# Optimization experiments

Hardware: AMD Instinct MI355X
Metric: run time of the kernel (lower is better)

The kernel has to match this reference:

```python
import jax, jax.numpy as jnp
import numpy as np

C = 128; D_INNER = 256; D_STATE = 16; D_CONV = 4; DT_RANK = 8; SCALE_MLP = 2


def layernorm(x, g, b, eps=1e-5):
    m = x.mean(-1, keepdims=True)
    v = ((x - m) ** 2).mean(-1, keepdims=True)
    return (x - m) * jax.lax.rsqrt(v + eps) * g + b


def causal_conv(x, w, b):
    # x: (B, L, D); w: (D, K) depthwise causal conv; b: (D,)
    K = w.shape[1]
    xt = x.transpose(0, 2, 1)  # (B, D, L)
    out = jax.lax.conv_general_dilated(
        xt, w[:, None, :], (1,), [(K - 1, 0)],
        dimension_numbers=("NCH", "OIH", "NCH"), feature_group_count=w.shape[0])
    return (out + b[None, :, None]).transpose(0, 2, 1)


def selective_scan(u, delta, A, Bm, Cm, Dv):
    # u, delta: (B, L, D); A: (D, N); Bm, Cm: (B, L, N); Dv: (D,)
    def step(h, inp):
        u_t, d_t, B_t, C_t = inp  # (B,D),(B,D),(B,N),(B,N)
        dA = jnp.exp(d_t[..., None] * A)                      # (B, D, N)
        h = dA * h + (d_t * u_t)[..., None] * B_t[:, None, :]  # (B, D, N)
        y = jnp.einsum("bdn,bn->bd", h, C_t)
        return h, y
    Bsz, L, Din = u.shape
    h0 = jnp.zeros((Bsz, Din, A.shape[1]), u.dtype)
    inputs = (u.transpose(1, 0, 2), delta.transpose(1, 0, 2),
              Bm.transpose(1, 0, 2), Cm.transpose(1, 0, 2))
    _, ys = jax.lax.scan(step, h0, inputs)
    return ys.transpose(1, 0, 2) + u * Dv


def mamba_branch(xc, z, cw, cb, Wx_, Wdt_, bdt_, Al, Dv):
    u = jax.nn.silu(causal_conv(xc, cw, cb))
    xdbl = u @ Wx_.T  # (B, L, dt_rank + 2*d_state)
    dr = Wdt_.shape[1]; ds = Al.shape[1]
    dt = jax.nn.softplus(xdbl[..., :dr] @ Wdt_.T + bdt_)
    Bm = xdbl[..., dr:dr + ds]
    Cm = xdbl[..., dr + ds:]
    y = selective_scan(u, dt, -jnp.exp(Al), Bm, Cm, Dv)
    return y * jax.nn.silu(z)


def setup_inputs():
    key = jax.random.key(0)
    ks = jax.random.split(key, 20)
    w = lambda k, shape, s=0.02: jax.random.normal(k, shape, jnp.float32) * s
    A_log = jnp.log(jnp.tile(jnp.arange(1, D_STATE + 1, dtype=jnp.float32), (D_INNER, 1)))
    dt_bias = jnp.full((D_INNER,), jnp.log(jnp.expm1(0.01)), jnp.float32)
    return dict(
        x=jax.random.normal(ks[0], (4, 256, 64, C), jnp.float32),
        g1=jnp.ones((C,), jnp.float32), b1=jnp.zeros((C,), jnp.float32),
        W_in=w(ks[1], (2 * D_INNER, C)),
        conv_w=w(ks[2], (D_INNER, D_CONV), 0.2), conv_b=jnp.zeros((D_INNER,), jnp.float32),
        Wx=w(ks[3], (DT_RANK + 2 * D_STATE, D_INNER)),
        Wdt=w(ks[4], (D_INNER, DT_RANK), 0.1), bdt=dt_bias,
        A_log=A_log, D=jnp.ones((D_INNER,), jnp.float32),
        conv_wb=w(ks[5], (D_INNER, D_CONV), 0.2), conv_bb=jnp.zeros((D_INNER,), jnp.float32),
        Wxb=w(ks[6], (DT_RANK + 2 * D_STATE, D_INNER)),
        Wdtb=w(ks[7], (D_INNER, DT_RANK), 0.1), bdtb=dt_bias,
        A_b_log=A_log, D_b=jnp.ones((D_INNER,), jnp.float32),
        W_out=w(ks[8], (C, D_INNER)),
        g2=jnp.ones((C,), jnp.float32), b2=jnp.zeros((C,), jnp.float32),
        g3=jnp.ones((C,), jnp.float32), b3=jnp.zeros((C,), jnp.float32),
        W1m=w(ks[9], (C, SCALE_MLP * C)), b1m=jnp.zeros((SCALE_MLP * C,), jnp.float32),
        W2m=w(ks[10], (SCALE_MLP * C, C)), b2m=jnp.zeros((C,), jnp.float32),
    )


def reference(x, g1, b1, W_in, conv_w, conv_b, Wx, Wdt, bdt, A_log, D,
              conv_wb, conv_bb, Wxb, Wdtb, bdtb, A_b_log, D_b, W_out,
              g2, b2, g3, b3, W1m, b1m, W2m, b2m):
    B, T, N, Cc = x.shape
    xs = x.transpose(0, 2, 1, 3).reshape(B * N, T, Cc)
    # --- CustomBiMamba: LN -> (Dropout eval=identity) -> BiMamba v2 -> LN, residual ---
    h = layernorm(xs, g1, b1)
    xz = h @ W_in.T  # (B*N, T, 2*d_inner)
    xc, z = jnp.split(xz, 2, axis=-1)
    y_f = mamba_branch(xc, z, conv_w, conv_b, Wx, Wdt, bdt, A_log, D)
    y_b = mamba_branch(xc[:, ::-1], z[:, ::-1], conv_wb, conv_bb, Wxb, Wdtb, bdtb,
                       A_b_log, D_b)[:, ::-1]
    y = (y_f + y_b) @ W_out.T
    y = layernorm(y, g2, b2)
    xs = y + xs
    xo = xs.reshape(B, N, T, Cc).transpose(0, 2, 1, 3)
    # --- MLP residual ---
    h2 = layernorm(xo, g3, b3)
    mlp = jax.nn.gelu(h2 @ W1m + b1m, approximate=False) @ W2m + b2m
    return xo + mlp
```

## Files before the change

kernel.cpp:

```cpp
#include <hip/hip_runtime.h>
#include <hip/hip_bf16.h>
#include <math.h>

#define CC 128
#define DI 256
#define SSEQ 256
#define ROWS 65536

typedef __hip_bfloat16 bf16;
typedef __attribute__((ext_vector_type(8))) short short8;
typedef __attribute__((ext_vector_type(4))) float float4v;
typedef __attribute__((ext_vector_type(2))) float f32x2;

__device__ __forceinline__ float to_f(float v) { return v; }
__device__ __forceinline__ float to_f(bf16 v)  { return __bfloat162float(v); }
__device__ __forceinline__ bf16  f2b(float v)  { return __float2bfloat16(v); }
__device__ __forceinline__ float bf2f_bits(short v) {
    union { unsigned u; float f; } c; c.u = ((unsigned)(unsigned short)v) << 16; return c.f;
}
__device__ __forceinline__ f32x2 mk2(float a, float b) { f32x2 r; r.x = a; r.y = b; return r; }
__device__ __forceinline__ f32x2 fma2(f32x2 a, f32x2 b, f32x2 c) { return a * b + c; }

__device__ __forceinline__ float wave_sum(float v) {
    #pragma unroll
    for (int o = 1; o < 64; o <<= 1) v += __shfl_xor(v, o, 64);
    return v;
}
__device__ __forceinline__ float silu_f(float x) {
    return x * __builtin_amdgcn_rcpf(1.f + __expf(-x));
}
__device__ __forceinline__ float gelu_f(float x) { return 0.5f * x * (1.f + erff(x * 0.70710678118654752f)); }
__device__ __forceinline__ float softplus_f(float x) {
    return (x > 20.f) ? x : __logf(1.f + __expf(x));
}

__global__ __launch_bounds__(256) void ln1_kernel(const float* __restrict__ x,
                                                  const float* __restrict__ g,
                                                  const float* __restrict__ b,
                                                  bf16* __restrict__ out) {
    int wave = threadIdx.x >> 6, lane = threadIdx.x & 63;
    int r = blockIdx.x * 4 + wave;
    int s = r >> 8, t = r & 255;
    int bb = s >> 6, n = s & 63;
    size_t xbase = (((size_t)(bb * 256 + t)) * 64 + n) * CC;
    float v0 = x[xbase + lane], v1 = x[xbase + lane + 64];
    float s1 = wave_sum(v0 + v1);
    float s2 = wave_sum(v0 * v0 + v1 * v1);
    float m = s1 * (1.f / 128.f);
    float var = s2 * (1.f / 128.f) - m * m;
    float rstd = rsqrtf(var + 1e-5f);
    size_t ob = (size_t)r * CC;
    out[ob + lane]      = f2b((v0 - m) * rstd * g[lane]      + b[lane]);
    out[ob + lane + 64] = f2b((v1 - m) * rstd * g[lane + 64] + b[lane + 64]);
}

template <bool BTR, int EPI, int KTILES>
__global__ __launch_bounds__(256) void mfma_gemm_kernel(const bf16* __restrict__ A, int lda,
                                                        const float* __restrict__ B,
                                                        const float* __restrict__ bias,
                                                        void* __restrict__ Cout, int ldc,
                                                        int N, int K) {
    __shared__ bf16 As[64][40];
    __shared__ bf16 Bs[64][40];
    int tid = threadIdx.x;
    int m0 = blockIdx.x * 64;
    int n0 = blockIdx.y * 64;
    int wv = tid >> 6, lane = tid & 63;
    int lrow = lane & 15, quad = lane >> 4;
    int lk = quad * 8;
    float4v acc[4] = {};
    #pragma unroll
    for (int kt = 0; kt < KTILES; kt++) {
        int k0 = kt * 32;
        {
            int m = tid >> 2, part = tid & 3;
            uint4 v = *(const uint4*)(A + (size_t)(m0 + m) * lda + k0 + part * 8);
            *(uint4*)&As[m][part * 8] = v;
        }
        if (BTR) {
            int n = tid >> 2, part = tid & 3;
            const float* src = B + (size_t)(n0 + n) * K + k0 + part * 8;
            bf16 tmp[8];
            #pragma unroll
            for (int j = 0; j < 8; j++) tmp[j] = f2b(src[j]);
            *(uint4*)&Bs[n][part * 8] = *(uint4*)tmp;
        } else {
            int kk = tid >> 3, nf = (tid & 7) * 8;
            const float* src = B + (size_t)(k0 + kk) * N + n0 + nf;
            #pragma unroll
            for (int j = 0; j < 8; j++) Bs[nf + j][kk] = f2b(src[j]);
        }
        __syncthreads();
        short8 a = *(const short8*)&As[wv * 16 + lrow][lk];
        #pragma unroll
        for (int jt = 0; jt < 4; jt++) {
            short8 bfr = *(const short8*)&Bs[jt * 16 + lrow][lk];
            acc[jt] = __builtin_amdgcn_mfma_f32_16x16x32_bf16(a, bfr, acc[jt], 0, 0, 0);
        }
        __syncthreads();
    }
    #pragma unroll
    for (int jt = 0; jt < 4; jt++) {
        int col = n0 + jt * 16 + lrow;
        float bs = (EPI >= 1) ? bias[col] : 0.f;
        #pragma unroll
        for (int r = 0; r < 4; r++) {
            int row = m0 + wv * 16 + quad * 4 + r;
            float v = acc[jt][r] + bs;
            if (EPI == 1) v = gelu_f(v);
            if (EPI == 2) {
                float* Cf = (float*)Cout;
                Cf[(size_t)row * ldc + col] += v;
            } else {
                bf16* Cb = (bf16*)Cout;
                Cb[(size_t)row * ldc + col] = f2b(v);
            }
        }
    }
}

__global__ __launch_bounds__(256) void mfma_ln2res_kernel(const bf16* __restrict__ YF,
                                                          const bf16* __restrict__ YB,
                                                          const bf16* __restrict__ xz,
                                                          const float* __restrict__ Wout,
                                                          const float* __restrict__ g,
                                                          const float* __restrict__ b,
                                                          const float* __restrict__ x,
                                                          float* __restrict__ out) {
    __shared__ bf16 As[64][40];
    __shared__ bf16 Bs[128][40];
    int tid = threadIdx.x;
    int m0 = blockIdx.x * 64;
    int wv = tid >> 6, lane = tid & 63;
    int lrow = lane & 15, quad = lane >> 4;
    int lk = quad * 8;
    float4v acc[8] = {};
    #pragma unroll
    for (int kt = 0; kt < 8; kt++) {
        int k0 = kt * 32;
        {
            int m = tid >> 2, part = tid & 3;
            size_t off = (size_t)(m0 + m) * 256 + k0 + part * 8;
            short8 vf = *(const short8*)(YF + off);
            short8 vb = *(const short8*)(YB + off);
            short8 vz = *(const short8*)(xz + (size_t)(m0 + m) * 512 + 256 + k0 + part * 8);
            bf16 tmp[8];
            #pragma unroll
            for (int j = 0; j < 8; j++)
                tmp[j] = f2b((bf2f_bits(vf[j]) + bf2f_bits(vb[j])) * silu_f(bf2f_bits(vz[j])));
            *(uint4*)&As[m][part * 8] = *(uint4*)tmp;
        }
        #pragma unroll
        for (int it = 0; it < 2; it++) {
            int idx = tid + it * 256;
            int n = idx >> 2, part = idx & 3;
            const float* src = Wout + (size_t)n * 256 + k0 + part * 8;
            bf16 tmp[8];
            #pragma unroll
            for (int j = 0; j < 8; j++) tmp[j] = f2b(src[j]);
            *(uint4*)&Bs[n][part * 8] = *(uint4*)tmp;
        }
        __syncthreads();
        short8 a = *(const short8*)&As[wv * 16 + lrow][lk];
        #pragma unroll
        for (int jt = 0; jt < 8; jt++) {
            short8 bfr = *(const short8*)&Bs[jt * 16 + lrow][lk];
            acc[jt] = __builtin_amdgcn_mfma_f32_16x16x32_bf16(a, bfr, acc[jt], 0, 0, 0);
        }
        __syncthreads();
    }
    #pragma unroll
    for (int r = 0; r < 4; r++) {
        float ps = 0.f, ps2 = 0.f;
        #pragma unroll
        for (int jt = 0; jt < 8; jt++) { float v = acc[jt][r]; ps += v; ps2 += v * v; }
        #pragma unroll
        for (int o = 1; o < 16; o <<= 1) {
            ps  += __shfl_xor(ps, o, 64);
            ps2 += __shfl_xor(ps2, o, 64);
        }
        float m = ps * (1.f / 128.f);
        float var = ps2 * (1.f / 128.f) - m * m;
        float rstd = rsqrtf(var + 1e-5f);
        int row = m0 + wv * 16 + quad * 4 + r;
        int s = row >> 8, t = row & 255;
        int bb = s >> 6, n = s & 63;
        size_t xbase = (((size_t)(bb * 256 + t)) * 64 + n) * CC;
        #pragma unroll
        for (int jt = 0; jt < 8; jt++) {
            int col = jt * 16 + lrow;
            out[xbase + col] = (acc[jt][r] - m) * rstd * g[col] + b[col] + x[xbase + col];
        }
    }
}

template <int DIR>
__global__ __launch_bounds__(256) void mfma_conv_kernel(const bf16* __restrict__ xz,
                                                        const float* __restrict__ cw,
                                                        const float* __restrict__ cb,
                                                        const float* __restrict__ Wx,
                                                        bf16* __restrict__ C,
                                                        bf16* __restrict__ U) {
    __shared__ bf16 As[64][40];
    __shared__ bf16 Bs[48][40];
    int tid = threadIdx.x;
    int s = blockIdx.x >> 2;
    int t0 = (blockIdx.x & 3) * 64;
    int wv = tid >> 6, lane = tid & 63;
    int lrow = lane & 15, quad = lane >> 4;
    int lk = quad * 8;
    float4v acc[3] = {};
    #pragma unroll
    for (int kt = 0; kt < 8; kt++) {
        int k0 = kt * 32;
        {
            int m = tid >> 2, part = tid & 3;
            int t = t0 + m;
            int dbase = k0 + part * 8;
            float a[8];
            float4 w4[8];
            #pragma unroll
            for (int i = 0; i < 8; i++) {
                a[i]  = cb[dbase + i];
                w4[i] = ((const float4*)cw)[dbase + i];
            }
            #pragma unroll
            for (int j = 0; j < 4; j++) {
                int tj = t - 3 + j;
                if (tj >= 0) {
                    int src = DIR ? (255 - tj) : tj;
                    uint4 v = *(const uint4*)(xz + (size_t)(s * 256 + src) * 512 + dbase);
                    short8 sv = *(short8*)&v;
                    #pragma unroll
                    for (int i = 0; i < 8; i++) {
                        float w = (j == 0) ? w4[i].x : (j == 1) ? w4[i].y : (j == 2) ? w4[i].z : w4[i].w;
                        a[i] += w * bf2f_bits(sv[i]);
                    }
                }
            }
            bf16 tmp[8];
            #pragma unroll
            for (int i = 0; i < 8; i++) tmp[i] = f2b(silu_f(a[i]));
            *(uint4*)&As[m][part * 8] = *(uint4*)tmp;
            int tu = DIR ? (255 - t) : t;
            *(uint4*)&U[((size_t)(s * 256 + tu)) * 256 + dbase] = *(uint4*)tmp;
        }
        {
            int n = tid >> 2, part = tid & 3;
            if (n < 48) {
                bf16 tmp[8];
                #pragma unroll
                for (int j = 0; j < 8; j++)
                    tmp[j] = (n < 40) ? f2b(Wx[(size_t)n * 256 + k0 + part * 8 + j]) : f2b(0.f);
                *(uint4*)&Bs[n][part * 8] = *(uint4*)tmp;
            }
        }
        __syncthreads();
        short8 a = *(const short8*)&As[wv * 16 + lrow][lk];
        #pragma unroll
        for (int jt = 0; jt < 3; jt++) {
            short8 bfr = *(const short8*)&Bs[jt * 16 + lrow][lk];
            acc[jt] = __builtin_amdgcn_mfma_f32_16x16x32_bf16(a, bfr, acc[jt], 0, 0, 0);
        }
        __syncthreads();
    }
    #pragma unroll
    for (int jt = 0; jt < 3; jt++) {
        int col = jt * 16 + lrow;
        if (col < 40) {
            #pragma unroll
            for (int r = 0; r < 4; r++) {
                int row = t0 + wv * 16 + quad * 4 + r;
                C[(size_t)(s * 256 + row) * 40 + col] = f2b(acc[jt][r]);
            }
        }
    }
}


#define LOADROW(R, T) do {                                                  \
    const float4* rp_ = (const float4*)(rows + (T) * 40);                   \
    R##0 = rp_[0]; R##1 = rp_[1]; R##2 = rp_[2]; R##3 = rp_[3];             \
    R##4 = rp_[4]; R##5 = rp_[5]; R##6 = rp_[6]; R##7 = rp_[7];             \
    R##8 = rp_[8]; R##9 = rp_[9];                                           \
} while (0)

#define SCAN_STEP(JJ, R) do {                                               \
    float u_ = to_f(ub[(JJ) * 256 + d]);                                    \
    f32x2 acc2 = mk2((R##0).x, (R##0).y) * wdt01;                           \
    acc2 = fma2(mk2((R##0).z, (R##0).w), wdt23, acc2);                      \
    acc2 = fma2(mk2((R##1).x, (R##1).y), wdt45, acc2);                      \
    acc2 = fma2(mk2((R##1).z, (R##1).w), wdt67, acc2);                      \
    float dtr_ = bd + acc2.x + acc2.y;                                      \
    float dt_ = softplus_f(dtr_);                                           \
    float du_ = dt_ * u_;                                                   \
    float d1 = __expf(dt_ * A0);                                            \
    float d2v = d1 * d1;                                                    \
    f32x2 pw0 = mk2(d1, d2v);                                               \
    f32x2 dd2 = mk2(d2v, d2v);                                              \
    f32x2 pw1 = pw0 * dd2, pw2 = pw1 * dd2, pw3 = pw2 * dd2;                \
    f32x2 dd8 = mk2(pw3.y, pw3.y);                                          \
    f32x2 pw4 = pw0 * dd8, pw5 = pw1 * dd8, pw6 = pw2 * dd8, pw7 = pw3 * dd8; \
    f32x2 du2 = mk2(du_, du_);                                              \
    hp0 = fma2(pw0, hp0, du2 * mk2((R##2).x, (R##2).y));                    \
    hp1 = fma2(pw1, hp1, du2 * mk2((R##2).z, (R##2).w));                    \
    hp2 = fma2(pw2, hp2, du2 * mk2((R##3).x, (R##3).y));                    \
    hp3 = fma2(pw3, hp3, du2 * mk2((R##3).z, (R##3).w));                    \
    hp4 = fma2(pw4, hp4, du2 * mk2((R##4).x, (R##4).y));                    \
    hp5 = fma2(pw5, hp5, du2 * mk2((R##4).z, (R##4).w));                    \
    hp6 = fma2(pw6, hp6, du2 * mk2((R##5).x, (R##5).y));                    \
    hp7 = fma2(pw7, hp7, du2 * mk2((R##5).z, (R##5).w));                    \
    f32x2 ya = hp0 * mk2((R##6).x, (R##6).y);                               \
    f32x2 yb2 = hp1 * mk2((R##6).z, (R##6).w);                              \
    ya = fma2(hp2, mk2((R##7).x, (R##7).y), ya);                            \
    yb2 = fma2(hp3, mk2((R##7).z, (R##7).w), yb2);                          \
    ya = fma2(hp4, mk2((R##8).x, (R##8).y), ya);                            \
    yb2 = fma2(hp5, mk2((R##8).z, (R##8).w), yb2);                          \
    ya = fma2(hp6, mk2((R##9).x, (R##9).y), ya);                            \
    yb2 = fma2(hp7, mk2((R##9).z, (R##9).w), yb2);                          \
    f32x2 ys = ya + yb2;                                                    \
    float yv_ = ys.x + ys.y + u_ * Dd;                                      \
    *yp = f2b(yv_); yp += ystep;                                            \
} while (0)

#define STAGE_U(BUF, C0) do {                                               \
    _Pragma("unroll")                                                       \
    for (int q_ = 0; q_ < 4; q_++) {                                        \
        int flat_ = q_ * 256 + tid;                                         \
        int j_ = flat_ >> 5, w_ = flat_ & 31;                               \
        int t_ = (C0) + j_;                                                 \
        int grow_ = dir ? (255 - t_) : t_;                                  \
        ((uint4*)u_lds)[(BUF) * 1024 + flat_] =                             \
            *((const uint4*)(Y + ((size_t)(s * 256 + grow_)) * 256) + w_);  \
    }                                                                       \
} while (0)

__global__ __launch_bounds__(256, 2) void scan_kernel(
        const bf16* __restrict__ xdbl_f, const bf16* __restrict__ xdbl_b,
        const float* __restrict__ Wdt_f, const float* __restrict__ bdt_f,
        const float* __restrict__ Alog_f, const float* __restrict__ D_f,
        const float* __restrict__ Wdt_b, const float* __restrict__ bdt_b,
        const float* __restrict__ Alog_b, const float* __restrict__ D_b,
        bf16* __restrict__ YF, bf16* __restrict__ YB) {
    __shared__ float rows[256 * 40];
    __shared__ bf16  u_lds[2 * 8192];
    int tid = threadIdx.x;
    int dir = blockIdx.x >> 8;
    int s = blockIdx.x & 255;
    int d = tid;

    const bf16* xd = (dir ? xdbl_b : xdbl_f) + (size_t)s * 10240;
    #pragma unroll
    for (int i = 0; i < 5; i++) {
        int idx = i * 256 + tid;
        uint4 v = ((const uint4*)xd)[idx];
        short8 sv = *(short8*)&v;
        float f[8];
        #pragma unroll
        for (int j = 0; j < 8; j++) f[j] = bf2f_bits(sv[j]);
        *(float4*)&rows[idx * 8]     = *(float4*)&f[0];
        *(float4*)&rows[idx * 8 + 4] = *(float4*)&f[4];
    }

    const float* Alog = dir ? Alog_b : Alog_f;
    const float* Wdtp = dir ? Wdt_b  : Wdt_f;
    float Aarr[16];
    #pragma unroll
    for (int n = 0; n < 16; n++) Aarr[n] = -__expf(Alog[d * 16 + n]);
    f32x2 wdt01 = mk2(Wdtp[d * 8 + 0], Wdtp[d * 8 + 1]);
    f32x2 wdt23 = mk2(Wdtp[d * 8 + 2], Wdtp[d * 8 + 3]);
    f32x2 wdt45 = mk2(Wdtp[d * 8 + 4], Wdtp[d * 8 + 5]);
    f32x2 wdt67 = mk2(Wdtp[d * 8 + 6], Wdtp[d * 8 + 7]);
    float bd = dir ? bdt_b[d] : bdt_f[d];
    float Dd = dir ? D_b[d]   : D_f[d];
    bf16* Y = dir ? YB : YF;

    float A0 = Aarr[0];
    int pw = 1;
    #pragma unroll
    for (int n = 1; n < 16; n++)
        pw &= (fabsf(Aarr[n] - (float)(n + 1) * A0) <= 1e-4f * fabsf(Aarr[n]) + 1e-6f) ? 1 : 0;
    pw = __all(pw);

    STAGE_U(0, 0);
    __syncthreads();

    bf16* yp = Y + ((size_t)(s * 256 + (dir ? 255 : 0))) * 256 + d;
    ptrdiff_t ystep = dir ? -256 : 256;

    if (pw) {
        f32x2 hp0 = {}, hp1 = {}, hp2 = {}, hp3 = {},
              hp4 = {}, hp5 = {}, hp6 = {}, hp7 = {};
        float4 ra0, ra1, ra2, ra3, ra4, ra5, ra6, ra7, ra8, ra9;
        float4 rb0, rb1, rb2, rb3, rb4, rb5, rb6, rb7, rb8, rb9;
        LOADROW(ra, 0);
        #pragma unroll 1
        for (int c = 0; c < 8; c++) {
            if (c + 1 < 8) STAGE_U((c + 1) & 1, (c + 1) * 32);
            const bf16* ub = u_lds + (c & 1) * 8192;
            int tc = c * 32;
            #pragma unroll 2
            for (int j = 0; j < 32; j += 2) {
                int t = tc + j;
                LOADROW(rb, t + 1);
                SCAN_STEP(j, ra);
                if (t + 2 < 256) LOADROW(ra, t + 2);
                SCAN_STEP(j + 1, rb);
            }
            __syncthreads();
        }
    } else {
        float h[16];
        #pragma unroll
        for (int n = 0; n < 16; n++) h[n] = 0.f;
        #pragma unroll 1
        for (int c = 0; c < 8; c++) {
            if (c + 1 < 8) STAGE_U((c + 1) & 1, (c + 1) * 32);
            const bf16* ub = u_lds + (c & 1) * 8192;
            int tc = c * 32;
            #pragma unroll 1
            for (int j = 0; j < 32; j++) {
                float u = to_f(ub[j * 256 + d]);
                const float* row = rows + (tc + j) * 40;
                float4 q0 = *(const float4*)(row);
                float4 q1 = *(const float4*)(row + 4);
                float dtr = bd;
                dtr += q0.x * wdt01.x + q0.y * wdt01.y + q0.z * wdt23.x + q0.w * wdt23.y;
                dtr += q1.x * wdt45.x + q1.y * wdt45.y + q1.z * wdt67.x + q1.w * wdt67.y;
                float dt = softplus_f(dtr);
                float du = dt * u, y = 0.f;
                #pragma unroll
                for (int n = 0; n < 16; n++) {
                    float dA = __expf(dt * Aarr[n]);
                    h[n] = dA * h[n] + du * row[8 + n];
                    y += h[n] * row[24 + n];
                }
                y += u * Dd;
                *yp = f2b(y); yp += ystep;
            }
            __syncthreads();
        }
    }
}

__global__ __launch_bounds__(256) void prep_w_kernel(const float* __restrict__ W1m,
                                                     const float* __restrict__ W2m,
                                                     bf16* __restrict__ W1T,
                                                     bf16* __restrict__ W2T) {
    int e = blockIdx.x * 256 + threadIdx.x;
    {
        int k = e >> 8, n = e & 255;
        W1T[n * 128 + k] = f2b(W1m[k * 256 + n]);
    }
    {
        int k = e >> 7, n = e & 127;
        W2T[n * 256 + k] = f2b(W2m[k * 128 + n]);
    }
}

__global__ __launch_bounds__(256) void mlp_fused_kernel(
        float* __restrict__ out,
        const float* __restrict__ g3, const float* __restrict__ b3,
        const bf16* __restrict__ W1T, const float* __restrict__ b1m,
        const bf16* __restrict__ W2T, const float* __restrict__ b2m) {
    __shared__ bf16 As[64][136];
    __shared__ bf16 Hs[64][264];
    __shared__ bf16 Bs[256][40];
    int tid = threadIdx.x;
    int m0 = blockIdx.x * 64;
    int wv = tid >> 6, lane = tid & 63;
    int lrow = lane & 15, quad = lane >> 4;
    int lk = quad * 8;

    {
        int m = tid >> 2, part = tid & 3;
        const float* src = out + (size_t)(m0 + m) * CC + part * 32;
        float v[32];
        #pragma unroll
        for (int i = 0; i < 8; i++) {
            float4 q = ((const float4*)src)[i];
            v[i * 4 + 0] = q.x; v[i * 4 + 1] = q.y;
            v[i * 4 + 2] = q.z; v[i * 4 + 3] = q.w;
        }
        float s1 = 0.f, s2 = 0.f;
        #pragma unroll
        for (int i = 0; i < 32; i++) { s1 += v[i]; s2 += v[i] * v[i]; }
        s1 += __shfl_xor(s1, 1, 64); s2 += __shfl_xor(s2, 1, 64);
        s1 += __shfl_xor(s1, 2, 64); s2 += __shfl_xor(s2, 2, 64);
        float mean = s1 * (1.f / 128.f);
        float var = s2 * (1.f / 128.f) - mean * mean;
        float rstd = rsqrtf(var + 1e-5f);
        #pragma unroll
        for (int i8 = 0; i8 < 4; i8++) {
            bf16 tmp[8];
            #pragma unroll
            for (int j = 0; j < 8; j++) {
                int col = part * 32 + i8 * 8 + j;
                tmp[j] = f2b((v[i8 * 8 + j] - mean) * rstd * g3[col] + b3[col]);
            }
            *(uint4*)&As[m][part * 32 + i8 * 8] = *(uint4*)tmp;
        }
    }
    __syncthreads();

    {
        float4v acc1[16] = {};
        #pragma unroll
        for (int kt = 0; kt < 4; kt++) {
            int k0 = kt * 32;
            #pragma unroll
            for (int it = 0; it < 4; it++) {
                int idx = tid + it * 256;
                int n = idx >> 2, part = idx & 3;
                *(uint4*)&Bs[n][part * 8] =
                    *(const uint4*)(W1T + (size_t)n * 128 + k0 + part * 8);
            }
            __syncthreads();
            short8 a = *(const short8*)&As[wv * 16 + lrow][k0 + lk];
            #pragma unroll
            for (int jt = 0; jt < 16; jt++) {
                short8 bfr = *(const short8*)&Bs[jt * 16 + lrow][lk];
                acc1[jt] = __builtin_amdgcn_mfma_f32_16x16x32_bf16(a, bfr, acc1[jt], 0, 0, 0);
            }
            __syncthreads();
        }
        #pragma unroll
        for (int jt = 0; jt < 16; jt++) {
            int col = jt * 16 + lrow;
            float bs = b1m[col];
            #pragma unroll
            for (int r = 0; r < 4; r++) {
                int row = wv * 16 + quad * 4 + r;
                Hs[row][col] = f2b(gelu_f(acc1[jt][r] + bs));
            }
        }
    }
    __syncthreads();

    float4v acc2[8] = {};
    #pragma unroll
    for (int kt = 0; kt < 8; kt++) {
        int k0 = kt * 32;
        #pragma unroll
        for (int it = 0; it < 2; it++) {
            int idx = tid + it * 256;
            int n = idx >> 2, part = idx & 3;
            *(uint4*)&Bs[n][part * 8] =
                *(const uint4*)(W2T + (size_t)n * 256 + k0 + part * 8);
        }
        __syncthreads();
        short8 a = *(const short8*)&Hs[wv * 16 + lrow][k0 + lk];
        #pragma unroll
        for (int jt = 0; jt < 8; jt++) {
            short8 bfr = *(const short8*)&Bs[jt * 16 + lrow][lk];
            acc2[jt] = __builtin_amdgcn_mfma_f32_16x16x32_bf16(a, bfr, acc2[jt], 0, 0, 0);
        }
        __syncthreads();
    }
    #pragma unroll
    for (int jt = 0; jt < 8; jt++) {
        int col = jt * 16 + lrow;
        float bs = b2m[col];
        #pragma unroll
        for (int r = 0; r < 4; r++) {
            int row = m0 + wv * 16 + quad * 4 + r;
            float* p = out + (size_t)row * CC + col;
            *p = *p + acc2[jt][r] + bs;
        }
    }
}

extern "C" void kernel_launch(void* const* d_in, const int* in_sizes, int n_in,
                              void* d_out, int out_size, void* d_ws, size_t ws_size,
                              hipStream_t stream) {
    const float* x      = (const float*)d_in[0];
    const float* g1     = (const float*)d_in[1];
    const float* b1     = (const float*)d_in[2];
    const float* W_in   = (const float*)d_in[3];
    const float* conv_w = (const float*)d_in[4];
    const float* conv_b = (const float*)d_in[5];
    const float* Wx     = (const float*)d_in[6];
    const float* Wdt    = (const float*)d_in[7];
    const float* bdt    = (const float*)d_in[8];
    const float* A_log  = (const float*)d_in[9];
    const float* Dvec   = (const float*)d_in[10];
    const float* conv_wb= (const float*)d_in[11];
    const float* conv_bb= (const float*)d_in[12];
    const float* Wxb    = (const float*)d_in[13];
    const float* Wdtb   = (const float*)d_in[14];
    const float* bdtb   = (const float*)d_in[15];
    const float* A_b_log= (const float*)d_in[16];
    const float* D_b    = (const float*)d_in[17];
    const float* W_out  = (const float*)d_in[18];
    const float* g2     = (const float*)d_in[19];
    const float* b2     = (const float*)d_in[20];
    const float* g3     = (const float*)d_in[21];
    const float* b3     = (const float*)d_in[22];
    const float* W1m    = (const float*)d_in[23];
    const float* b1m    = (const float*)d_in[24];
    const float* W2m    = (const float*)d_in[25];
    const float* b2m    = (const float*)d_in[26];

    bf16* ws  = (bf16*)d_ws;
    bf16* XZ  = ws;
    bf16* YF  = ws + 33554432UL;
    bf16* YB  = ws + 50331648UL;
    float* out = (float*)d_out;
    bf16* LN1OUT = (bf16*)d_out;
    bf16* XDBL_F = (bf16*)d_out;
    bf16* XDBL_B = (bf16*)d_out + 2621440UL;
    bf16* W1T = XZ;
    bf16* W2T = XZ + 32768UL;

    ln1_kernel<<<ROWS / 4, 256, 0, stream>>>(x, g1, b1, LN1OUT);
    mfma_gemm_kernel<true, 0, 4><<<dim3(ROWS / 64, 8), 256, 0, stream>>>(
        LN1OUT, CC, W_in, nullptr, XZ, 512, 512, CC);
    mfma_conv_kernel<0><<<SSEQ * 4, 256, 0, stream>>>(XZ, conv_w, conv_b, Wx, XDBL_F, YF);
    mfma_conv_kernel<1><<<SSEQ * 4, 256, 0, stream>>>(XZ, conv_wb, conv_bb, Wxb, XDBL_B, YB);
    scan_kernel<<<512, 256, 0, stream>>>(XDBL_F, XDBL_B,
        Wdt, bdt, A_log, Dvec, Wdtb, bdtb, A_b_log, D_b, YF, YB);
    mfma_ln2res_kernel<<<ROWS / 64, 256, 0, stream>>>(YF, YB, XZ, W_out, g2, b2, x, out);
    prep_w_kernel<<<128, 256, 0, stream>>>(W1m, W2m, W1T, W2T);
    mlp_fused_kernel<<<ROWS / 64, 256, 0, stream>>>(out, g3, b3, W1T, b1m, W2T, b2m);
}
```

Baseline: 460.7 us.

## Fuse LayerNorm1 into W_in projection GEMM kernel

Replaces the separate LN1 kernel and the tiled input-projection GEMM with one kernel. Each block normalizes 64 rows into shared memory with the full K=128 resident, then loops over all 8 output column tiles, reusing the A tile. This removes the bf16 LN1 round trip through global memory and one launch. In exchange each block serially converts all of W_in and loops over N, so there is less parallelism per launch, and stores to XZ remain scattered 2-byte writes.

```diff
diff --git a/kernel.cpp b/kernel.cpp
--- a/kernel.cpp
+++ b/kernel.cpp
@@ -34,88 +34,87 @@
     return (x > 20.f) ? x : __logf(1.f + __expf(x));
 }
 
-__global__ __launch_bounds__(256) void ln1_kernel(const float* __restrict__ x,
-                                                  const float* __restrict__ g,
-                                                  const float* __restrict__ b,
-                                                  bf16* __restrict__ out) {
-    int wave = threadIdx.x >> 6, lane = threadIdx.x & 63;
-    int r = blockIdx.x * 4 + wave;
-    int s = r >> 8, t = r & 255;
-    int bb = s >> 6, n = s & 63;
-    size_t xbase = (((size_t)(bb * 256 + t)) * 64 + n) * CC;
-    float v0 = x[xbase + lane], v1 = x[xbase + lane + 64];
-    float s1 = wave_sum(v0 + v1);
-    float s2 = wave_sum(v0 * v0 + v1 * v1);
-    float m = s1 * (1.f / 128.f);
-    float var = s2 * (1.f / 128.f) - m * m;
-    float rstd = rsqrtf(var + 1e-5f);
-    size_t ob = (size_t)r * CC;
-    out[ob + lane]      = f2b((v0 - m) * rstd * g[lane]      + b[lane]);
-    out[ob + lane + 64] = f2b((v1 - m) * rstd * g[lane + 64] + b[lane + 64]);
-}
-
-template <bool BTR, int EPI, int KTILES>
-__global__ __launch_bounds__(256) void mfma_gemm_kernel(const bf16* __restrict__ A, int lda,
-                                                        const float* __restrict__ B,
-                                                        const float* __restrict__ bias,
-                                                        void* __restrict__ Cout, int ldc,
-                                                        int N, int K) {
-    __shared__ bf16 As[64][40];
-    __shared__ bf16 Bs[64][40];
+__global__ __launch_bounds__(256) void ln1_win_kernel(
+        const float* __restrict__ x,
+        const float* __restrict__ g, const float* __restrict__ b,
+        const float* __restrict__ Win,
+        bf16* __restrict__ XZ) {
+    __shared__ bf16 As[64][136];
+    __shared__ bf16 Bs[64][136];
     int tid = threadIdx.x;
     int m0 = blockIdx.x * 64;
-    int n0 = blockIdx.y * 64;
     int wv = tid >> 6, lane = tid & 63;
     int lrow = lane & 15, quad = lane >> 4;
     int lk = quad * 8;
-    float4v acc[4] = {};
-    #pragma unroll
-    for (int kt = 0; kt < KTILES; kt++) {
-        int k0 = kt * 32;
+
+    {
+        int m = tid >> 2, part = tid & 3;
+        int r = m0 + m;
+        int s = r >> 8, t = r & 255;
+        int bb = s >> 6, nn = s & 63;
+        const float* src = x + (((size_t)(bb * 256 + t)) * 64 + nn) * CC + part * 32;
+        float v[32];
+        #pragma unroll
+        for (int i = 0; i < 8; i++) {
+            float4 q = ((const float4*)src)[i];
+            v[i * 4 + 0] = q.x; v[i * 4 + 1] = q.y;
+            v[i * 4 + 2] = q.z; v[i * 4 + 3] = q.w;
+        }
+        float s1 = 0.f, s2 = 0.f;
+        #pragma unroll
+        for (int i = 0; i < 32; i++) { s1 += v[i]; s2 += v[i] * v[i]; }
+        s1 += __shfl_xor(s1, 1, 64); s2 += __shfl_xor(s2, 1, 64);
+        s1 += __shfl_xor(s1, 2, 64); s2 += __shfl_xor(s2, 2, 64);
+        float mean = s1 * (1.f / 128.f);
+        float var = s2 * (1.f / 128.f) - mean * mean;
+        float rstd = rsqrtf(var + 1e-5f);
+        #pragma unroll
+        for (int i8 = 0; i8 < 4; i8++) {
+            bf16 tmp[8];
+            #pragma unroll
+            for (int j = 0; j < 8; j++) {
+                int col = part * 32 + i8 * 8 + j;
+                tmp[j] = f2b((v[i8 * 8 + j] - mean) * rstd * g[col] + b[col]);
+            }
+            *(uint4*)&As[m][part * 32 + i8 * 8] = *(uint4*)tmp;
+        }
+    }
+    __syncthreads();
+
+    #pragma unroll 1
+    for (int nt = 0; nt < 8; nt++) {
         {
-            int m = tid >> 2, part = tid & 3;
-            uint4 v = *(const uint4*)(A + (size_t)(m0 + m) * lda + k0 + part * 8);
-            *(uint4*)&As[m][part * 8] = v;
-        }
-        if (BTR) {
             int n = tid >> 2, part = tid & 3;
-            const float* src = B + (size_t)(n0 + n) * K + k0 + part * 8;
-            bf16 tmp[8];
-            #pragma unroll
-            for (int j = 0; j < 8; j++) tmp[j] = f2b(src[j]);
-            *(uint4*)&Bs[n][part * 8] = *(uint4*)tmp;
-        } else {
-            int kk = tid >> 3, nf = (tid & 7) * 8;
-            const float* src = B + (size_t)(k0 + kk) * N + n0 + nf;
-            #pragma unroll
-            for (int j = 0; j < 8; j++) Bs[nf + j][kk] = f2b(src[j]);
-        }
-        __syncthreads();
-        short8 a = *(const short8*)&As[wv * 16 + lrow][lk];
+            const float* srcB = Win + ((size_t)(nt * 64 + n)) * CC + part * 32;
+            #pragma unroll
+            for (int i8 = 0; i8 < 4; i8++) {
+                bf16 tmp[8];
+                #pragma unroll
+                for (int j = 0; j < 8; j++) tmp[j] = f2b(srcB[i8 * 8 + j]);
+                *(uint4*)&Bs[n][part * 32 + i8 * 8] = *(uint4*)tmp;
+            }
+        }
+        __syncthreads();
+        float4v acc[4] = {};
+        #pragma unroll
+        for (int kt = 0; kt < 4; kt++) {
+            short8 a = *(const short8*)&As[wv * 16 + lrow][kt * 32 + lk];
+            #pragma unroll
+            for (int jt = 0; jt < 4; jt++) {
+                short8 bfr = *(const short8*)&Bs[jt * 16 + lrow][kt * 32 + lk];
+                acc[jt] = __builtin_amdgcn_mfma_f32_16x16x32_bf16(a, bfr, acc[jt], 0, 0, 0);
+            }
+        }
         #pragma unroll
         for (int jt = 0; jt < 4; jt++) {
-            short8 bfr = *(const short8*)&Bs[jt * 16 + lrow][lk];
-            acc[jt] = __builtin_amdgcn_mfma_f32_16x16x32_bf16(a, bfr, acc[jt], 0, 0, 0);
-        }
-        __syncthreads();
-    }
-    #pragma unroll
-    for (int jt = 0; jt < 4; jt++) {
-        int col = n0 + jt * 16 + lrow;
-        float bs = (EPI >= 1) ? bias[col] : 0.f;
-        #pragma unroll
-        for (int r = 0; r < 4; r++) {
-            int row = m0 + wv * 16 + quad * 4 + r;
-            float v = acc[jt][r] + bs;
-            if (EPI == 1) v = gelu_f(v);
-            if (EPI == 2) {
-                float* Cf = (float*)Cout;
-                Cf[(size_t)row * ldc + col] += v;
-            } else {
-                bf16* Cb = (bf16*)Cout;
-                Cb[(size_t)row * ldc + col] = f2b(v);
-            }
-        }
+            int col = nt * 64 + jt * 16 + lrow;
+            #pragma unroll
+            for (int r = 0; r < 4; r++) {
+                int row = m0 + wv * 16 + quad * 4 + r;
+                XZ[(size_t)row * 512 + col] = f2b(acc[jt][r]);
+            }
+        }
+        __syncthreads();
     }
 }
 
@@ -606,15 +605,12 @@
     bf16* YF  = ws + 33554432UL;
     bf16* YB  = ws + 50331648UL;
     float* out = (float*)d_out;
-    bf16* LN1OUT = (bf16*)d_out;
     bf16* XDBL_F = (bf16*)d_out;
     bf16* XDBL_B = (bf16*)d_out + 2621440UL;
     bf16* W1T = XZ;
     bf16* W2T = XZ + 32768UL;
 
-    ln1_kernel<<<ROWS / 4, 256, 0, stream>>>(x, g1, b1, LN1OUT);
-    mfma_gemm_kernel<true, 0, 4><<<dim3(ROWS / 64, 8), 256, 0, stream>>>(
-        LN1OUT, CC, W_in, nullptr, XZ, 512, 512, CC);
+    ln1_win_kernel<<<ROWS / 64, 256, 0, stream>>>(x, g1, b1, W_in, XZ);
     mfma_conv_kernel<0><<<SSEQ * 4, 256, 0, stream>>>(XZ, conv_w, conv_b, Wx, XDBL_F, YF);
     mfma_conv_kernel<1><<<SSEQ * 4, 256, 0, stream>>>(XZ, conv_wb, conv_bb, Wxb, XDBL_B, YB);
     scan_kernel<<<512, 256, 0, stream>>>(XDBL_F, XDBL_B,
```

New measurement: 472.1 us. +2.5%, slower.
